# Kernel tuning notes

Measured on AMD Instinct MI355X. Metric: run time of the kernel, lower is better.

## Reference

```python
import jax, jax.numpy as jnp
import numpy as np

AMBIENT = [2, 2, 2]
DEGREES = [a + 1 for a in AMBIENT]          # coords per projective factor
N_COORDS = sum(DEGREES)                      # 9
STARTS = np.concatenate([[0], np.cumsum(DEGREES)[:-1]])
CONST_MULT = 1.0
CLIP = 1.0e6


def _get_real_imag_of_prod(cp):
    """cp: complex [B, n]. Returns (real [B, n(n+1)/2], imag [B, n(n-1)/2]).
    Matches TF boolean_mask(transpose(...)) ordering: row-major (b, a) with b<=a;
    real = (XX+YY)[x, b, a] (symmetric), imag = +XY_YX[x, b, a] for b<a."""
    X, Y = jnp.real(cp), jnp.imag(cp)
    XX_YY = jnp.einsum('xa,xb->xab', X, X) + jnp.einsum('xa,xb->xab', Y, Y)
    XY = jnp.einsum('xa,xb->xab', X, Y)
    XY_YX = XY - XY.transpose(0, 2, 1)      # antisymmetric
    n = cp.shape[1]
    iu = jnp.triu_indices(n)                # incl. diagonal
    su = jnp.triu_indices(n, 1)             # strict upper
    real = XX_YY[:, iu[0], iu[1]]
    imag = XY_YX[:, su[0], su[1]]
    return real, imag


def _bihom(points):
    """points: complex [B, N_COORDS] -> real [B, 729] section products / kappa."""
    B = points.shape[0]
    kappas_prod = jnp.ones((B,), points.real.dtype)
    it_r = it_i = None
    for i, (s, d) in enumerate(zip(STARTS, DEGREES)):
        cp = points[:, s:s + d]
        kappas_prod = kappas_prod * jnp.sum(jnp.abs(cp) ** 2, axis=-1)
        r, im = _get_real_imag_of_prod(cp)
        if i == 0:
            it_r, it_i = r, im
        else:
            new_r = jnp.concatenate([
                jnp.einsum('bi,bj->bij', it_r, r).reshape(B, -1),
                -jnp.einsum('bi,bj->bij', it_i, im).reshape(B, -1)], axis=1)
            new_i = jnp.concatenate([
                jnp.einsum('bi,bj->bij', it_r, im).reshape(B, -1),
                -jnp.einsum('bi,bj->bij', it_i, r).reshape(B, -1)], axis=1)
            it_r, it_i = new_r, new_i
    sec = jnp.concatenate([it_r, it_i], axis=-1)
    return sec / kappas_prod[:, None]


def _tower(h, W1, b1, W2, b2, W3, b3, Wf):
    # Dense layers with square activation, then log|.| into bias-free final Dense
    h = (h @ W1 + b1) ** 2
    h = (h @ W2 + b2) ** 2
    h = (h @ W3 + b3) ** 2
    return jnp.log(jnp.abs(h)) @ Wf


def setup_inputs() -> dict:
    key = jax.random.key(0)
    ks = jax.random.split(key, 16)
    B = 32768
    s = 0.05
    inp = {
        'x':   jax.random.normal(ks[0], (B, 2 * N_COORDS), jnp.float32),
        'W1a': jax.random.normal(ks[1], (729, 1024), jnp.float32) * s,
        'b1a': jax.random.normal(ks[2], (1024,), jnp.float32) * s,
        'W2a': jax.random.normal(ks[3], (1024, 1024), jnp.float32) * s,
        'b2a': jax.random.normal(ks[4], (1024,), jnp.float32) * s,
        'W3a': jax.random.normal(ks[5], (1024, 1), jnp.float32) * s,
        'b3a': jax.random.normal(ks[6], (1,), jnp.float32) * s,
        'Wfa': jnp.ones((1, 1), jnp.float32),
        'W1b': jax.random.normal(ks[7], (729, 1024), jnp.float32) * s,
        'b1b': jax.random.normal(ks[8], (1024,), jnp.float32) * s,
        'W2b': jax.random.normal(ks[9], (1024, 1024), jnp.float32) * s,
        'b2b': jax.random.normal(ks[10], (1024,), jnp.float32) * s,
        'W3b': jax.random.normal(ks[11], (1024, 1), jnp.float32) * s,
        'b3b': jax.random.normal(ks[12], (1,), jnp.float32) * s,
        'Wfb': jnp.ones((1, 1), jnp.float32),
    }
    return inp


def reference(x, W1a, b1a, W2a, b2a, W3a, b3a, Wfa,
              W1b, b1b, W2b, b2b, W3b, b3b, Wfb):
    points = jax.lax.complex(x[:, :N_COORDS], x[:, N_COORDS:])
    feats = _bihom(points)                     # [B, 729]
    out = _tower(feats, W1a, b1a, W2a, b2a, W3a, b3a, Wfa) \
        - _tower(feats, W1b, b1b, W2b, b2b, W3b, b3b, Wfb)
    return CONST_MULT * jnp.clip(out, -CLIP, CLIP)
```

## Files before the change

kernel.cpp:

```cpp
#include <hip/hip_runtime.h>

typedef unsigned short u16;
typedef unsigned int u32;
typedef __attribute__((ext_vector_type(8))) short bf16x8;
typedef __attribute__((ext_vector_type(4))) float f32x4;

__device__ __forceinline__ u16 f2bf(float x){
  unsigned u = __builtin_bit_cast(unsigned, x);
  unsigned r = (u + 0x7FFFu + ((u >> 16) & 1u)) >> 16;
  return (u16)r;
}
__device__ __forceinline__ float bf2f(u16 h){
  unsigned u = ((unsigned)h) << 16;
  return __builtin_bit_cast(float, u);
}

__device__ __forceinline__ void gld_lds16(const void* g, void* l){
  __builtin_amdgcn_global_load_lds((const __attribute__((address_space(1))) void*)g,
                                   (__attribute__((address_space(3))) void*)l,
                                   16, 0, 0);
}

__global__ void wconv_kernel(const float* __restrict__ W0, u16* __restrict__ Th0, int K0p,
                             const float* __restrict__ W1, u16* __restrict__ Th1, int K1p,
                             const float* __restrict__ W2, u16* __restrict__ Th2, int K2p,
                             const float* __restrict__ W3, u16* __restrict__ Th3, int K3p)
{
  __shared__ float t[32][33];
  int z = blockIdx.z;
  const float* W = z==0 ? W0 : z==1 ? W1 : z==2 ? W2 : W3;
  u16* Th = z==0 ? Th0 : z==1 ? Th1 : z==2 ? Th2 : Th3;
  int Kpad = z==0 ? K0p : z==1 ? K1p : z==2 ? K2p : K3p;
  int K = (Kpad == 768) ? 729 : 1024;
  int k0 = blockIdx.x * 32;
  if (k0 >= Kpad) return;
  int n0 = blockIdx.y * 32;
  int tx = threadIdx.x & 31, ty = threadIdx.x >> 5;
#pragma unroll
  for (int j = 0; j < 4; j++){
    int k = k0 + ty + j*8;
    float v = (k < K) ? W[(size_t)k*1024 + (n0 + tx)] : 0.f;
    t[ty + j*8][tx] = v;
  }
  __syncthreads();
#pragma unroll
  for (int j = 0; j < 4; j++){
    int n = n0 + ty + j*8;
    int k = k0 + tx;
    size_t idx = (size_t)n*Kpad + k;
    Th[idx] = f2bf(t[tx][ty + j*8]);
  }
}

__global__ void feats_kernel(const float* __restrict__ x,
                             u16* __restrict__ fh,
                             int row0)
{
  __shared__ float cC[8][28];
  __shared__ float tA[8][81];
  __shared__ float tB[8][12];
  __shared__ float ivk[8];
  const int tid = threadIdx.x;
  const int lrow0 = blockIdx.x * 8;
  if (tid < 8){
    const float* xr = x + (size_t)(row0 + lrow0 + tid) * 18;
    float kk = 1.f;
#pragma unroll
    for (int f = 0; f < 3; f++){
      float xa = xr[3*f+0], xb = xr[3*f+1], xc = xr[3*f+2];
      float ya = xr[9+3*f+0], yb = xr[9+3*f+1], yc = xr[9+3*f+2];
      int bse = f * 9;
      cC[tid][bse+0] = xa*xa + ya*ya;
      cC[tid][bse+1] = xa*xb + ya*yb;
      cC[tid][bse+2] = xa*xc + ya*yc;
      cC[tid][bse+3] = xb*xb + yb*yb;
      cC[tid][bse+4] = xb*xc + yb*yc;
      cC[tid][bse+5] = xc*xc + yc*yc;
      cC[tid][bse+6] = xa*yb - xb*ya;
      cC[tid][bse+7] = xa*yc - xc*ya;
      cC[tid][bse+8] = xb*yc - xc*yb;
      kk *= (xa*xa+ya*ya + xb*xb+yb*yb + xc*xc+yc*yc);
    }
    ivk[tid] = 1.f / kk;
#pragma unroll
    for (int j = 0; j < 6; j++) tB[tid][j] = cC[tid][18+j];
#pragma unroll
    for (int j = 0; j < 3; j++) tB[tid][6+j] = cC[tid][24+j];
  }
  __syncthreads();
#pragma unroll 1
  for (int e = tid; e < 648; e += 256){
    int r = e / 81;
    int k = e - r*81;
    const float* cc = cC[r];
    float val;
    if (k < 36)      {               val =   cc[k/6]     * cc[9  + k%6]; }
    else if (k < 45) { int u = k-36; val = -(cc[6 + u/3] * cc[15 + u%3]); }
    else if (k < 63) { int u = k-45; val =   cc[u/3]     * cc[15 + u%3]; }
    else             { int u = k-63; val = -(cc[6 + u/6] * cc[9  + u%6]); }
    tA[r][k] = val;
  }
  __syncthreads();
#pragma unroll 1
  for (int jj = 0; jj < 3; jj++){
    int o = jj*256 + tid;
    int idxA = 0, idxB = 0; float sgn = 0.f;
    if (o < 270)      {              idxA = o/6;      idxB = o - (o/6)*6; sgn =  1.f; }
    else if (o < 378) { int t = o-270; idxA = 45 + t/3; idxB = 6 + t%3;   sgn = -1.f; }
    else if (o < 513) { int t = o-378; idxA = t/3;      idxB = 6 + t%3;   sgn =  1.f; }
    else if (o < 729) { int t = o-513; idxA = 45 + t/6; idxB = t%6;       sgn = -1.f; }
#pragma unroll
    for (int r = 0; r < 8; r++){
      float v = sgn * tA[r][idxA] * tB[r][idxB] * ivk[r];
      size_t oi = (size_t)(lrow0 + r) * 768 + o;
      fh[oi] = f2bf(v);
    }
  }
}

#define GEMM_SMEM_BYTES (49152*2 + 4096)

#define STAGE(BUF) do{ \
    u16* _a = sA + (BUF)*8192; u16* _b = sB + (BUF)*8192; \
    gld_lds16(gAh0, _a + wave*1024); gld_lds16(gAh1, _a + wave*1024 + 512); \
    gld_lds16(gBh0, _b + wave*1024); gld_lds16(gBh1, _b + wave*1024 + 512); \
    gAh0 += 32; gAh1 += 32; gBh0 += 32; gBh1 += 32; \
  }while(0)

#define BARRIER()  asm volatile("s_barrier" ::: "memory")

template<int MODE>
__global__ __launch_bounds__(512, 1) void gemm_k(
    const u16* __restrict__ Ahi,
    const u16* __restrict__ Bhi,
    const float* __restrict__ bias,
    u16* __restrict__ Oh,
    const float* __restrict__ W3, float* __restrict__ P, int Pstride,
    int K)
{
  extern __shared__ __align__(16) u16 smem[];
  u16* sA = smem;
  u16* sB = smem + 24576;
  float* rowsum = (float*)(smem + 49152);

  const int nwg = gridDim.x;
  const int qq = nwg >> 3;
  const int wg = (nwg & 7) ? (int)blockIdx.x
                           : ((blockIdx.x & 7) * qq + (blockIdx.x >> 3));
  const int nb = wg & 3;
  const int mb = wg >> 2;

  const int tid = threadIdx.x;
  const int wave = tid >> 6, lane = tid & 63;
  const int wm = wave >> 2, wn = wave & 3;

  const int l4 = lane >> 2, ls = lane & 3;
  const int fsw  = (l4 >> 1) & 3;
  const int koff = ((ls ^ fsw) << 3);

  const u16* gAh0 = Ahi + (size_t)(mb*256 + wave*32 + l4) * K + koff;
  const u16* gAh1 = gAh0 + (size_t)16 * K;
  const u16* gBh0 = Bhi + (size_t)(nb*256 + wave*32 + l4) * K + koff;
  const u16* gBh1 = gBh0 + (size_t)16 * K;

  const int r16 = lane & 15, g = lane >> 4;
  const int fr   = (r16 >> 1) & 3;
  const int slot = ((g ^ fr) << 3);

  f32x4 acc[8][4];
#pragma unroll
  for (int m = 0; m < 8; m++)
#pragma unroll
    for (int n = 0; n < 4; n++)
      acc[m][n] = (f32x4){0.f, 0.f, 0.f, 0.f};

  const int NT = K >> 5;
  STAGE(0); STAGE(1);

#pragma unroll 1
  for (int t = 0; t < NT; ++t){
    if (t + 1 < NT){
      asm volatile("s_waitcnt vmcnt(4)" ::: "memory");
    } else {
      asm volatile("s_waitcnt vmcnt(0)" ::: "memory");
    }
    BARRIER();
    if (t + 2 < NT){
      int b2 = (t + 2) % 3;
      STAGE(b2);
    }
    const int cur = t % 3;
    const u16* pA = sA + cur*8192;
    const u16* pB = sB + cur*8192;
    bf16x8 ah[8], bh[4];
#pragma unroll
    for (int n = 0; n < 4; n++) bh[n] = *(const bf16x8*)(pB + (wn*64 + n*16 + r16)*32 + slot);
#pragma unroll
    for (int m = 0; m < 8; m++) ah[m] = *(const bf16x8*)(pA + (wm*128 + m*16 + r16)*32 + slot);
    __builtin_amdgcn_s_setprio(1);
#pragma unroll
    for (int m = 0; m < 8; m++)
#pragma unroll
      for (int n = 0; n < 4; n++)
        acc[m][n] = __builtin_amdgcn_mfma_f32_16x16x32_bf16(ah[m], bh[n], acc[m][n], 0, 0, 0);
    __builtin_amdgcn_s_setprio(0);
  }

  if constexpr (MODE == 0){
#pragma unroll
    for (int n = 0; n < 4; n++){
      int col = nb*256 + wn*64 + n*16 + r16;
      float bv = bias[col];
#pragma unroll
      for (int m = 0; m < 8; m++){
        int rbase = mb*256 + wm*128 + m*16 + g*4;
#pragma unroll
        for (int q = 0; q < 4; q++){
          float val = acc[m][n][q] + bv;
          val = val * val;
          size_t oi = (size_t)(rbase + q) * 1024 + col;
          Oh[oi] = f2bf(val);
        }
      }
    }
  } else {
    float w3v[4], bv[4];
#pragma unroll
    for (int n = 0; n < 4; n++){
      int col = nb*256 + wn*64 + n*16 + r16;
      w3v[n] = W3[col];
      bv[n]  = bias[col];
    }
    float rp[8][4];
#pragma unroll
    for (int m = 0; m < 8; m++)
#pragma unroll
      for (int q = 0; q < 4; q++)
        rp[m][q] = 0.f;
#pragma unroll
    for (int m = 0; m < 8; m++)
#pragma unroll
      for (int n = 0; n < 4; n++)
#pragma unroll
        for (int q = 0; q < 4; q++){
          float v = acc[m][n][q] + bv[n];
          rp[m][q] += v * v * w3v[n];
        }
#pragma unroll
    for (int m = 0; m < 8; m++)
#pragma unroll
      for (int q = 0; q < 4; q++){
        float s = rp[m][q];
        s += __shfl_xor(s, 1); s += __shfl_xor(s, 2);
        s += __shfl_xor(s, 4); s += __shfl_xor(s, 8);
        rp[m][q] = s;
      }
    if (r16 == 0){
#pragma unroll
      for (int m = 0; m < 8; m++)
#pragma unroll
        for (int q = 0; q < 4; q++)
          rowsum[wn*256 + wm*128 + m*16 + g*4 + q] = rp[m][q];
    }
    __syncthreads();
    if (tid < 256){
      float s = rowsum[tid] + rowsum[256 + tid] + rowsum[512 + tid] + rowsum[768 + tid];
      P[(size_t)nb * Pstride + mb*256 + tid] = s;
    }
  }
}

__global__ void finalize_kernel(const float* __restrict__ Pa, const float* __restrict__ Pb,
                                int Pstride,
                                const float* __restrict__ b3a, const float* __restrict__ Wfa,
                                const float* __restrict__ b3b, const float* __restrict__ Wfb,
                                float* __restrict__ out, int row0, int Rc)
{
  int r = blockIdx.x * 256 + threadIdx.x;
  if (r >= Rc) return;
  float sa = b3a[0], sb = b3b[0];
#pragma unroll
  for (int j = 0; j < 4; j++){
    sa += Pa[(size_t)j * Pstride + r];
    sb += Pb[(size_t)j * Pstride + r];
  }
  float ta = 2.f * logf(fabsf(sa)) * Wfa[0];
  float tb = 2.f * logf(fabsf(sb)) * Wfb[0];
  float o = ta - tb;
  o = fminf(fmaxf(o, -1000000.f), 1000000.f);
  out[row0 + r] = o;
}

static inline size_t align256(size_t v){ return (v + 255) & ~(size_t)255; }

extern "C" void kernel_launch(void* const* d_in, const int* in_sizes, int n_in,
                              void* d_out, int out_size, void* d_ws, size_t ws_size,
                              hipStream_t stream)
{
  (void)n_in; (void)out_size;
  const float* x   = (const float*)d_in[0];
  const float* W1a = (const float*)d_in[1];
  const float* b1a = (const float*)d_in[2];
  const float* W2a = (const float*)d_in[3];
  const float* b2a = (const float*)d_in[4];
  const float* W3a = (const float*)d_in[5];
  const float* b3a = (const float*)d_in[6];
  const float* Wfa = (const float*)d_in[7];
  const float* W1b = (const float*)d_in[8];
  const float* b1b = (const float*)d_in[9];
  const float* W2b = (const float*)d_in[10];
  const float* b2b = (const float*)d_in[11];
  const float* W3b = (const float*)d_in[12];
  const float* b3b = (const float*)d_in[13];
  const float* Wfb = (const float*)d_in[14];
  float* out = (float*)d_out;

  const int B  = in_sizes[0] / 18;
  const int K1 = 768;
  const int K2 = 1024;

  hipFuncSetAttribute((const void*)gemm_k<0>,
                      hipFuncAttributeMaxDynamicSharedMemorySize, GEMM_SMEM_BYTES);
  hipFuncSetAttribute((const void*)gemm_k<1>,
                      hipFuncAttributeMaxDynamicSharedMemorySize, GEMM_SMEM_BYTES);

  char* base = (char*)d_ws;
  size_t off = 0;
  auto carve = [&](size_t bytes) -> char* {
    off = align256(off);
    char* p = base + off;
    off += bytes;
    return p;
  };

  u16* wt1a = (u16*)carve((size_t)1024 * K1 * 2);
  u16* wt2a = (u16*)carve((size_t)1024 * K2 * 2);
  u16* wt1b = (u16*)carve((size_t)1024 * K1 * 2);
  u16* wt2b = (u16*)carve((size_t)1024 * K2 * 2);

  size_t fixed = align256(off);
  const long long per_row = (long long)K1*2 + 2048 + 32;
  long long avail = (long long)ws_size - (long long)fixed - 8192;
  long long rmax = avail > 0 ? avail / per_row : 0;
  int R = (int)((rmax / 256) * 256);
  if (R > B) R = B;
  if (R < 256) R = 256;

  u16* fh  = (u16*)carve((size_t)R * K1 * 2);
  u16* h1h = (u16*)carve((size_t)R * 1024 * 2);
  float* pa = (float*)carve((size_t)4 * R * 4);
  float* pb = (float*)carve((size_t)4 * R * 4);

  wconv_kernel<<<dim3(32, 32, 4), 256, 0, stream>>>(
      W1a, wt1a, K1,
      W2a, wt2a, K2,
      W1b, wt1b, K1,
      W2b, wt2b, K2);

  for (int row0 = 0; row0 < B; row0 += R){
    int Rc = B - row0; if (Rc > R) Rc = R;
    int MB = Rc / 256;
    feats_kernel<<<Rc/8, 256, 0, stream>>>(x, fh, row0);
    gemm_k<0><<<dim3(4*MB), 512, GEMM_SMEM_BYTES, stream>>>(
        fh, wt1a, b1a, h1h, nullptr, nullptr, 0, K1);
    gemm_k<1><<<dim3(4*MB), 512, GEMM_SMEM_BYTES, stream>>>(
        h1h, wt2a, b2a, nullptr, W3a, pa, R, K2);
    gemm_k<0><<<dim3(4*MB), 512, GEMM_SMEM_BYTES, stream>>>(
        fh, wt1b, b1b, h1h, nullptr, nullptr, 0, K1);
    gemm_k<1><<<dim3(4*MB), 512, GEMM_SMEM_BYTES, stream>>>(
        h1h, wt2b, b2b, nullptr, W3b, pb, R, K2);
    finalize_kernel<<<(Rc + 255)/256, 256, 0, stream>>>(pa, pb, R, b3a, Wfa, b3b, Wfb,
                                                        out, row0, Rc);
  }
}
```

Before: 285.6 us.

## Merge both towers into single GEMM launches and stage epilogue stores through LDS

Both towers' layer-1 GEMMs now run in one launch, and both layer-2 GEMMs in another, with the tower picked from the workgroup index. This doubles the grid per launch, cuts the launch count and tail effects, and lets the two towers share the fh input in cache. Each tower gets its own h1 buffer, which raises workspace per row and may shrink the row chunk R. The MODE 0 epilogue now writes bf16 results to LDS per wave and then issues 16-byte coalesced global stores instead of scattered 2-byte stores.

```diff
diff --git a/kernel.cpp b/kernel.cpp
--- a/kernel.cpp
+++ b/kernel.cpp
@@ -4,6 +4,8 @@
 typedef unsigned int u32;
 typedef __attribute__((ext_vector_type(8))) short bf16x8;
 typedef __attribute__((ext_vector_type(4))) float f32x4;
+typedef __attribute__((ext_vector_type(2))) unsigned int u32x2;
+typedef __attribute__((ext_vector_type(4))) unsigned int u32x4;
 
 __device__ __forceinline__ u16 f2bf(float x){
   unsigned u = __builtin_bit_cast(unsigned, x);
@@ -128,14 +130,16 @@
   }while(0)
 
 #define BARRIER()  asm volatile("s_barrier" ::: "memory")
+#define LGKM0()    asm volatile("s_waitcnt lgkmcnt(0)" ::: "memory")
 
 template<int MODE>
 __global__ __launch_bounds__(512, 1) void gemm_k(
-    const u16* __restrict__ Ahi,
-    const u16* __restrict__ Bhi,
-    const float* __restrict__ bias,
-    u16* __restrict__ Oh,
-    const float* __restrict__ W3, float* __restrict__ P, int Pstride,
+    const u16* __restrict__ Aa, const u16* __restrict__ Ab,
+    const u16* __restrict__ Ba, const u16* __restrict__ Bb,
+    const float* __restrict__ biasa, const float* __restrict__ biasb,
+    u16* __restrict__ Oa, u16* __restrict__ Ob,
+    const float* __restrict__ W3a_, const float* __restrict__ W3b_,
+    float* __restrict__ Pa, float* __restrict__ Pb, int Pstride,
     int K)
 {
   extern __shared__ __align__(16) u16 smem[];
@@ -148,7 +152,12 @@
   const int wg = (nwg & 7) ? (int)blockIdx.x
                            : ((blockIdx.x & 7) * qq + (blockIdx.x >> 3));
   const int nb = wg & 3;
-  const int mb = wg >> 2;
+  const int tower = (wg >> 2) & 1;
+  const int mb = wg >> 3;
+
+  const u16* Ahi = tower ? Ab : Aa;
+  const u16* Bhi = tower ? Bb : Ba;
+  const float* bias = tower ? biasb : biasa;
 
   const int tid = threadIdx.x;
   const int wave = tid >> 6, lane = tid & 63;
@@ -207,23 +216,40 @@
   }
 
   if constexpr (MODE == 0){
-#pragma unroll
-    for (int n = 0; n < 4; n++){
-      int col = nb*256 + wn*64 + n*16 + r16;
-      float bv = bias[col];
-#pragma unroll
-      for (int m = 0; m < 8; m++){
-        int rbase = mb*256 + wm*128 + m*16 + g*4;
+    u16* Oh = tower ? Ob : Oa;
+    float bv[4];
+#pragma unroll
+    for (int n = 0; n < 4; n++) bv[n] = bias[nb*256 + wn*64 + n*16 + r16];
+    __syncthreads();
+    u16* wbuf = smem + wave*1088;
+    const int rr = lane >> 2, c4 = lane & 3;
+#pragma unroll 1
+    for (int m = 0; m < 8; m++){
+#pragma unroll
+      for (int n = 0; n < 4; n++)
 #pragma unroll
         for (int q = 0; q < 4; q++){
-          float val = acc[m][n][q] + bv;
+          float val = acc[m][n][q] + bv[n];
           val = val * val;
-          size_t oi = (size_t)(rbase + q) * 1024 + col;
-          Oh[oi] = f2bf(val);
+          wbuf[(g*4 + q)*68 + n*16 + r16] = f2bf(val);
         }
-      }
+      LGKM0();
+      const u16* rp = wbuf + rr*68 + c4*16;
+      u32x2 d0 = *(const u32x2*)(rp);
+      u32x2 d1 = *(const u32x2*)(rp + 4);
+      u32x2 d2 = *(const u32x2*)(rp + 8);
+      u32x2 d3 = *(const u32x2*)(rp + 12);
+      size_t grow = (size_t)(mb*256 + wm*128 + m*16 + rr);
+      u16* gp = Oh + grow*1024 + nb*256 + wn*64 + c4*16;
+      u32x4 s0 = (u32x4){d0[0], d0[1], d1[0], d1[1]};
+      u32x4 s1 = (u32x4){d2[0], d2[1], d3[0], d3[1]};
+      *(u32x4*)(gp)     = s0;
+      *(u32x4*)(gp + 8) = s1;
+      LGKM0();
     }
   } else {
+    const float* W3 = tower ? W3b_ : W3a_;
+    float* P = tower ? Pb : Pa;
     float w3v[4], bv[4];
 #pragma unroll
     for (int n = 0; n < 4; n++){
@@ -339,15 +365,16 @@
   u16* wt2b = (u16*)carve((size_t)1024 * K2 * 2);
 
   size_t fixed = align256(off);
-  const long long per_row = (long long)K1*2 + 2048 + 32;
+  const long long per_row = (long long)K1*2 + 4096 + 64;
   long long avail = (long long)ws_size - (long long)fixed - 8192;
   long long rmax = avail > 0 ? avail / per_row : 0;
   int R = (int)((rmax / 256) * 256);
   if (R > B) R = B;
   if (R < 256) R = 256;
 
-  u16* fh  = (u16*)carve((size_t)R * K1 * 2);
-  u16* h1h = (u16*)carve((size_t)R * 1024 * 2);
+  u16* fh   = (u16*)carve((size_t)R * K1 * 2);
+  u16* h1a  = (u16*)carve((size_t)R * 1024 * 2);
+  u16* h1b  = (u16*)carve((size_t)R * 1024 * 2);
   float* pa = (float*)carve((size_t)4 * R * 4);
   float* pb = (float*)carve((size_t)4 * R * 4);
 
@@ -361,14 +388,12 @@
     int Rc = B - row0; if (Rc > R) Rc = R;
     int MB = Rc / 256;
     feats_kernel<<<Rc/8, 256, 0, stream>>>(x, fh, row0);
-    gemm_k<0><<<dim3(4*MB), 512, GEMM_SMEM_BYTES, stream>>>(
-        fh, wt1a, b1a, h1h, nullptr, nullptr, 0, K1);
-    gemm_k<1><<<dim3(4*MB), 512, GEMM_SMEM_BYTES, stream>>>(
-        h1h, wt2a, b2a, nullptr, W3a, pa, R, K2);
-    gemm_k<0><<<dim3(4*MB), 512, GEMM_SMEM_BYTES, stream>>>(
-        fh, wt1b, b1b, h1h, nullptr, nullptr, 0, K1);
-    gemm_k<1><<<dim3(4*MB), 512, GEMM_SMEM_BYTES, stream>>>(
-        h1h, wt2b, b2b, nullptr, W3b, pb, R, K2);
+    gemm_k<0><<<dim3(8*MB), 512, GEMM_SMEM_BYTES, stream>>>(
+        fh, fh, wt1a, wt1b, b1a, b1b,
+        h1a, h1b, nullptr, nullptr, nullptr, nullptr, 0, K1);
+    gemm_k<1><<<dim3(8*MB), 512, GEMM_SMEM_BYTES, stream>>>(
+        h1a, h1b, wt2a, wt2b, b2a, b2b,
+        nullptr, nullptr, W3a, W3b, pa, pb, R, K2);
     finalize_kernel<<<(Rc + 255)/256, 256, 0, stream>>>(pa, pb, R, b3a, Wfa, b3b, Wfb,
                                                         out, row0, Rc);
   }
```

After: 392.6 us. +37.5%, slower.
